# Kernel optimization log

Hardware: AMD Instinct MI355X
Metric: run time of the kernel (lower is better)

## Reference

```python
import jax, jax.numpy as jnp
import numpy as np

N = 262144
C = 256
G = 4096  # number of segments (upper bound on group ids)


def setup_inputs() -> dict:
    key = jax.random.key(0)
    ks = jax.random.split(key, 8)
    s = 1.0 / np.sqrt(C)
    x = jax.random.normal(ks[0], (1, N, C), dtype=jnp.float32)
    ix = jax.random.randint(ks[1], (N,), 0, G, dtype=jnp.int64)
    Wf = jax.random.uniform(ks[2], (C, C), jnp.float32, -s, s)
    bf = jax.random.uniform(ks[3], (C,), jnp.float32, -s, s)
    Wg = jax.random.uniform(ks[4], (C, C), jnp.float32, -s, s)
    bg = jax.random.uniform(ks[5], (C,), jnp.float32, -s, s)
    Wh = jax.random.uniform(ks[6], (C, C), jnp.float32, -s, s)
    bh = jax.random.uniform(ks[7], (C,), jnp.float32, -s, s)
    return {"x": x, "Wf": Wf, "bf": bf, "Wg": Wg, "bg": bg, "Wh": Wh, "bh": bh, "ix": ix}


def reference(x, Wf, bf, Wg, bg, Wh, bh, ix):
    # x: [1, N, C]; only batch 0 is used (matches torch module)
    x0 = x[0]                                    # [N, C]
    fx = x0 @ Wf.T + bf                          # [N, C]
    gx = jnp.clip(x0 @ Wg.T + bg, -50.0, 50.0)   # [N, C]
    exp_gx = jnp.exp(gx)                         # [N, C]
    # Segment softmax: sorting + cumsum group relabel in the torch code is
    # mathematically just a per-group normalized weighted sum keyed by ix.
    seg = ix.astype(jnp.int32)
    denom = jax.ops.segment_sum(exp_gx, seg, num_segments=G)   # [G, C]
    w = exp_gx / denom[seg]                                    # [N, C]
    y = jax.ops.segment_sum(fx * w, seg, num_segments=G)       # [G, C]
    y = y @ Wh.T + bh                                          # [G, C]
    out = y[seg]                                               # [N, C]
    return out[None]                                           # [1, N, C]
```

## Files before the change

kernel.cpp:

```cpp
#include <hip/hip_runtime.h>
#include <stdint.h>
#include <stddef.h>

#define N_ROWS 262144
#define CCH    256
#define NGRP   4096

typedef short bf16x8 __attribute__((ext_vector_type(8)));
typedef short bf16x4 __attribute__((ext_vector_type(4)));
typedef float f32x4  __attribute__((ext_vector_type(4)));
typedef int   i32x4  __attribute__((ext_vector_type(4)));

static __device__ __forceinline__ short f2bf(float f){
  union { float f; unsigned u; } v; v.f = f;
  unsigned u = v.u;
  unsigned r = (u + 0x7FFFu + ((u >> 16) & 1u)) >> 16;
  return (short)r;
}

typedef __attribute__((address_space(1))) const unsigned int GU32;
typedef __attribute__((address_space(3))) unsigned int LU32;
static __device__ __forceinline__ void gload_lds16(const void* g, void* l){
  __builtin_amdgcn_global_load_lds((GU32*)g, (LU32*)l, 16, 0, 0);
}

__global__ __launch_bounds__(256) void k_castw(
    const float* __restrict__ Wf, const float* __restrict__ Wg,
    const float* __restrict__ Wh,
    short* __restrict__ wfb, short* __restrict__ wgb, float* __restrict__ wht)
{
  int e = blockIdx.x * 256 + threadIdx.x;
  wfb[e] = f2bf(Wf[e]);
  wgb[e] = f2bf(Wg[e]);
  int k = e >> 8, j = e & 255;
  wht[e] = Wh[j * 256 + k];
}

__global__ __launch_bounds__(256) void k_hist(const int* __restrict__ ix, int* __restrict__ counts){
  int i = blockIdx.x * blockDim.x + threadIdx.x;
  int stride = gridDim.x * blockDim.x;
  for (; i < N_ROWS; i += stride) atomicAdd(&counts[ix[i]], 1);
}

__global__ __launch_bounds__(1024) void k_scan(const int* __restrict__ counts, int* __restrict__ cursor){
  __shared__ int sums[1024];
  int t = threadIdx.x;
  int base = t * 4;
  int c0 = counts[base], c1 = counts[base+1], c2 = counts[base+2], c3 = counts[base+3];
  sums[t] = c0 + c1 + c2 + c3;
  __syncthreads();
  for (int off = 1; off < 1024; off <<= 1){
    int v = (t >= off) ? sums[t - off] : 0;
    __syncthreads();
    sums[t] += v;
    __syncthreads();
  }
  int prev = (t == 0) ? 0 : sums[t - 1];
  cursor[base]   = prev;
  cursor[base+1] = prev + c0;
  cursor[base+2] = prev + c0 + c1;
  cursor[base+3] = prev + c0 + c1 + c2;
}

__global__ __launch_bounds__(256) void k_scatter(const int* __restrict__ ix, int* __restrict__ cursor,
                                                 int* __restrict__ order, int* __restrict__ gid){
  int i = blockIdx.x * blockDim.x + threadIdx.x;
  int stride = gridDim.x * blockDim.x;
  for (; i < N_ROWS; i += stride){
    int g = ix[i];
    int p = atomicAdd(&cursor[g], 1);
    order[p] = i;
    gid[p] = g;
  }
}

__global__ __launch_bounds__(256) void k_gemm(
    const float* __restrict__ x,
    const short* __restrict__ wfb, const short* __restrict__ wgb,
    const float* __restrict__ bfp, const float* __restrict__ bgp,
    const int* __restrict__ order, const int* __restrict__ gid,
    float* __restrict__ numer, float* __restrict__ denom)
{
  __shared__ short bst[2][2][8][512];
  __shared__ int ord_s[128];
  __shared__ int gid_s[128];

  const int tid  = threadIdx.x;
  const int wave = tid >> 6;
  const int lane = tid & 63;
  const int l16  = lane & 15;
  const int quad = lane >> 4;

  const int r0 = blockIdx.x * 128;
  const int j0 = blockIdx.y * 128;

  if (tid < 128){ ord_s[tid] = order[r0 + tid]; gid_s[tid] = gid[r0 + tid]; }
  __syncthreads();

  const float* xr0 = x + (size_t)ord_s[wave * 32 + l16] * 256;
  const float* xr1 = x + (size_t)ord_s[wave * 32 + 16 + l16] * 256;

  const int sm  = wave >> 1;
  const int sks = wave & 1;
  const short* wsrc = sm ? wgb : wfb;
  const short* bsrc = wsrc + (size_t)(j0 + l16) * 256 + sks * 32 + quad * 8;

  f32x4 accF[2][8], accG[2][8];
  #pragma unroll
  for (int rg = 0; rg < 2; ++rg)
    #pragma unroll
    for (int t = 0; t < 8; ++t){
      accF[rg][t] = (f32x4){0.f,0.f,0.f,0.f};
      accG[rg][t] = (f32x4){0.f,0.f,0.f,0.f};
    }

  for (int kc = 0; kc < 4; ++kc){
    const int k0 = kc * 64;
    #pragma unroll
    for (int t = 0; t < 8; ++t)
      gload_lds16(bsrc + (size_t)t * 16 * 256 + k0, &bst[sm][sks][t][0]);
    f32x4 av[2][2][2];
    #pragma unroll
    for (int rg = 0; rg < 2; ++rg){
      const float* xp = (rg ? xr1 : xr0) + k0 + quad * 8;
      #pragma unroll
      for (int ks = 0; ks < 2; ++ks){
        av[rg][ks][0] = *(const f32x4*)(xp + ks * 32);
        av[rg][ks][1] = *(const f32x4*)(xp + ks * 32 + 4);
      }
    }
    __syncthreads();
    #pragma unroll
    for (int ks = 0; ks < 2; ++ks){
      bf16x8 a0, a1;
      #pragma unroll
      for (int j = 0; j < 4; ++j){
        a0[j]   = f2bf(av[0][ks][0][j]);
        a0[4+j] = f2bf(av[0][ks][1][j]);
        a1[j]   = f2bf(av[1][ks][0][j]);
        a1[4+j] = f2bf(av[1][ks][1][j]);
      }
      #pragma unroll
      for (int t = 0; t < 8; ++t){
        bf16x8 bFv = *(const bf16x8*)&bst[0][ks][t][lane * 8];
        accF[0][t] = __builtin_amdgcn_mfma_f32_16x16x32_bf16(a0, bFv, accF[0][t], 0, 0, 0);
        accF[1][t] = __builtin_amdgcn_mfma_f32_16x16x32_bf16(a1, bFv, accF[1][t], 0, 0, 0);
        bf16x8 bGv = *(const bf16x8*)&bst[1][ks][t][lane * 8];
        accG[0][t] = __builtin_amdgcn_mfma_f32_16x16x32_bf16(a0, bGv, accG[0][t], 0, 0, 0);
        accG[1][t] = __builtin_amdgcn_mfma_f32_16x16x32_bf16(a1, bGv, accG[1][t], 0, 0, 0);
      }
    }
    __syncthreads();
  }

  float bfr[8], bgr[8];
  #pragma unroll
  for (int t = 0; t < 8; ++t){
    bfr[t] = bfp[j0 + t * 16 + l16];
    bgr[t] = bgp[j0 + t * 16 + l16];
  }
  #pragma unroll
  for (int rg = 0; rg < 2; ++rg)
    #pragma unroll
    for (int t = 0; t < 8; ++t)
      #pragma unroll
      for (int r = 0; r < 4; ++r){
        float g = accG[rg][t][r] + bgr[t];
        g = fminf(fmaxf(g, -50.f), 50.f);
        float e = __expf(g);
        accF[rg][t][r] = (accF[rg][t][r] + bfr[t]) * e;
        accG[rg][t][r] = e;
      }

  const int base = wave * 32;
  const int qd4 = quad * 4;
  int start = 0;
  while (start < 32){
    int g = gid_s[base + start];
    int end = start + 1;
    while (end < 32 && gid_s[base + end] == g) ++end;
    #pragma unroll
    for (int t = 0; t < 8; ++t){
      float sF = 0.f, sE = 0.f;
      #pragma unroll
      for (int rg = 0; rg < 2; ++rg)
        #pragma unroll
        for (int r = 0; r < 4; ++r){
          int rl = rg * 16 + qd4 + r;
          bool in = (rl >= start) && (rl < end);
          sF += in ? accF[rg][t][r] : 0.f;
          sE += in ? accG[rg][t][r] : 0.f;
        }
      sF += __shfl_xor(sF, 16); sF += __shfl_xor(sF, 32);
      sE += __shfl_xor(sE, 16); sE += __shfl_xor(sE, 32);
      if (quad == 0){
        atomicAdd(&numer[(size_t)g * 256 + j0 + t * 16 + l16], sF);
        atomicAdd(&denom[(size_t)g * 256 + j0 + t * 16 + l16], sE);
      }
    }
    start = end;
  }
}

__global__ __launch_bounds__(256) void k_yh(
    const float* __restrict__ numer, const float* __restrict__ denom,
    const float* __restrict__ wht, const float* __restrict__ bh,
    float* __restrict__ yh)
{
  __shared__ float ys[16][256];
  int t = threadIdx.x;
  int g0 = blockIdx.x * 16;
  #pragma unroll
  for (int gg = 0; gg < 16; ++gg){
    size_t idx = (size_t)(g0 + gg) * 256 + t;
    float d = denom[idx];
    ys[gg][t] = (d != 0.f) ? (numer[idx] / d) : 0.f;
  }
  __syncthreads();
  float acc[16];
  #pragma unroll
  for (int gg = 0; gg < 16; ++gg) acc[gg] = 0.f;
  for (int k = 0; k < 256; k += 4){
    float w0 = wht[(k+0) * 256 + t];
    float w1 = wht[(k+1) * 256 + t];
    float w2 = wht[(k+2) * 256 + t];
    float w3 = wht[(k+3) * 256 + t];
    #pragma unroll
    for (int gg = 0; gg < 16; ++gg)
      acc[gg] += w0 * ys[gg][k] + w1 * ys[gg][k+1] + w2 * ys[gg][k+2] + w3 * ys[gg][k+3];
  }
  float b = bh[t];
  #pragma unroll
  for (int gg = 0; gg < 16; ++gg) yh[(size_t)(g0 + gg) * 256 + t] = acc[gg] + b;
}

__global__ __launch_bounds__(256) void k_out(const int* __restrict__ ix,
    const float* __restrict__ yh, float* __restrict__ out)
{
  int wave = threadIdx.x >> 6;
  int lane = threadIdx.x & 63;
  int i = blockIdx.x * 4 + wave;
  int stride = gridDim.x * 4;
  for (; i < N_ROWS; i += stride){
    int g = ix[i];
    f32x4 v = *(const f32x4*)(yh + (size_t)g * 256 + lane * 4);
    *(f32x4*)(out + (size_t)i * 256 + lane * 4) = v;
  }
}

extern "C" void kernel_launch(void* const* d_in, const int* in_sizes, int n_in,
                              void* d_out, int out_size, void* d_ws, size_t ws_size,
                              hipStream_t stream)
{
  const float* x  = (const float*)d_in[0];
  const float* Wf = (const float*)d_in[1];
  const float* bf = (const float*)d_in[2];
  const float* Wg = (const float*)d_in[3];
  const float* bg = (const float*)d_in[4];
  const float* Wh = (const float*)d_in[5];
  const float* bh = (const float*)d_in[6];
  const int*   ix = (const int*)d_in[7];
  float* out = (float*)d_out;

  char* ws = (char*)d_ws;
  float* numer  = (float*)(ws + 0);
  float* denom  = (float*)(ws + 4194304);
  int*   counts = (int*)  (ws + 8388608);
  int*   cursor = (int*)  (ws + 8404992);
  float* yh     = (float*)(ws + 8421376);
  float* wht    = (float*)(ws + 12615680);
  short* wfb    = (short*)(ws + 12877824);
  short* wgb    = (short*)(ws + 13008896);
  int*   order  = (int*)  (ws + 13139968);
  int*   gid    = (int*)  (ws + 14188544);

  hipMemsetAsync(ws, 0, 8404992, stream);

  k_castw<<<256, 256, 0, stream>>>(Wf, Wg, Wh, wfb, wgb, wht);
  k_hist<<<512, 256, 0, stream>>>(ix, counts);
  k_scan<<<1, 1024, 0, stream>>>(counts, cursor);
  k_scatter<<<512, 256, 0, stream>>>(ix, cursor, order, gid);
  dim3 ggrid(2048, 2);
  k_gemm<<<ggrid, 256, 0, stream>>>(x, wfb, wgb, bf, bg, order, gid, numer, denom);
  k_yh<<<256, 256, 0, stream>>>(numer, denom, wht, bh, yh);
  k_out<<<2048, 256, 0, stream>>>(ix, yh, out);
}
```

Baseline: 850.7 us.

## Fuse row permutation with bf16 cast and make GEMM persistent with resident weights

The scatter kernel now writes each x row, already cast to bf16, into its sorted position in a scratch buffer that reuses the output allocation. The GEMM then reads contiguous bf16 rows instead of gathering fp32 rows through an index array. The GEMM becomes persistent: 512-thread blocks each keep a 64-column slice of both weight matrices in LDS for the whole run and loop over row tiles, which removes the per-k-chunk weight reloads and barriers. In exchange there is an extra pass writing the bf16 copy of x, plus more blocks hitting the same atomics, and correctness depends on k_out fully overwriting the output buffer afterwards.

Result: slower. 1.060 ms (+24.7%).

```diff
diff --git a/kernel.cpp b/kernel.cpp
--- a/kernel.cpp
+++ b/kernel.cpp
@@ -9,7 +9,6 @@
 typedef short bf16x8 __attribute__((ext_vector_type(8)));
 typedef short bf16x4 __attribute__((ext_vector_type(4)));
 typedef float f32x4  __attribute__((ext_vector_type(4)));
-typedef int   i32x4  __attribute__((ext_vector_type(4)));
 
 static __device__ __forceinline__ short f2bf(float f){
   union { float f; unsigned u; } v; v.f = f;
@@ -62,28 +61,36 @@
   cursor[base+3] = prev + c0 + c1 + c2;
 }
 
-__global__ __launch_bounds__(256) void k_scatter(const int* __restrict__ ix, int* __restrict__ cursor,
-                                                 int* __restrict__ order, int* __restrict__ gid){
-  int i = blockIdx.x * blockDim.x + threadIdx.x;
-  int stride = gridDim.x * blockDim.x;
+__global__ __launch_bounds__(256) void k_scatter_cast(
+    const int* __restrict__ ix, int* __restrict__ cursor,
+    const float* __restrict__ x, short* __restrict__ xb, int* __restrict__ gid)
+{
+  int wave = threadIdx.x >> 6;
+  int lane = threadIdx.x & 63;
+  int i = blockIdx.x * 4 + wave;
+  int stride = gridDim.x * 4;
   for (; i < N_ROWS; i += stride){
     int g = ix[i];
-    int p = atomicAdd(&cursor[g], 1);
-    order[p] = i;
-    gid[p] = g;
-  }
-}
-
-__global__ __launch_bounds__(256) void k_gemm(
-    const float* __restrict__ x,
+    int p;
+    if (lane == 0) p = atomicAdd(&cursor[g], 1);
+    p = __shfl(p, 0);
+    f32x4 v = *(const f32x4*)(x + (size_t)i * 256 + lane * 4);
+    bf16x4 b;
+    #pragma unroll
+    for (int j = 0; j < 4; ++j) b[j] = f2bf(v[j]);
+    *(bf16x4*)(xb + (size_t)p * 256 + lane * 4) = b;
+    if (lane == 0) gid[p] = g;
+  }
+}
+
+__global__ __launch_bounds__(512, 4) void k_gemm(
+    const short* __restrict__ xb,
     const short* __restrict__ wfb, const short* __restrict__ wgb,
     const float* __restrict__ bfp, const float* __restrict__ bgp,
-    const int* __restrict__ order, const int* __restrict__ gid,
+    const int* __restrict__ gid,
     float* __restrict__ numer, float* __restrict__ denom)
 {
-  __shared__ short bst[2][2][8][512];
-  __shared__ int ord_s[128];
-  __shared__ int gid_s[128];
+  __shared__ short bst[64][512];
 
   const int tid  = threadIdx.x;
   const int wave = tid >> 6;
@@ -91,114 +98,105 @@
   const int l16  = lane & 15;
   const int quad = lane >> 4;
 
-  const int r0 = blockIdx.x * 128;
-  const int j0 = blockIdx.y * 128;
-
-  if (tid < 128){ ord_s[tid] = order[r0 + tid]; gid_s[tid] = gid[r0 + tid]; }
+  const int cg    = blockIdx.x & 3;
+  const int bslot = blockIdx.x >> 2;
+  const int j0    = cg * 64;
+
+  #pragma unroll
+  for (int q = 0; q < 8; ++q){
+    int f = wave * 8 + q;
+    int mat = f >> 5, ks = (f >> 2) & 7, t = f & 3;
+    const short* wsrc = mat ? wgb : wfb;
+    const short* src = wsrc + (size_t)(j0 + t * 16 + l16) * 256 + ks * 32 + quad * 8;
+    gload_lds16(src, &bst[f][0]);
+  }
   __syncthreads();
 
-  const float* xr0 = x + (size_t)ord_s[wave * 32 + l16] * 256;
-  const float* xr1 = x + (size_t)ord_s[wave * 32 + 16 + l16] * 256;
-
-  const int sm  = wave >> 1;
-  const int sks = wave & 1;
-  const short* wsrc = sm ? wgb : wfb;
-  const short* bsrc = wsrc + (size_t)(j0 + l16) * 256 + sks * 32 + quad * 8;
-
-  f32x4 accF[2][8], accG[2][8];
-  #pragma unroll
-  for (int rg = 0; rg < 2; ++rg)
-    #pragma unroll
-    for (int t = 0; t < 8; ++t){
-      accF[rg][t] = (f32x4){0.f,0.f,0.f,0.f};
-      accG[rg][t] = (f32x4){0.f,0.f,0.f,0.f};
-    }
-
-  for (int kc = 0; kc < 4; ++kc){
-    const int k0 = kc * 64;
-    #pragma unroll
-    for (int t = 0; t < 8; ++t)
-      gload_lds16(bsrc + (size_t)t * 16 * 256 + k0, &bst[sm][sks][t][0]);
-    f32x4 av[2][2][2];
-    #pragma unroll
-    for (int rg = 0; rg < 2; ++rg){
-      const float* xp = (rg ? xr1 : xr0) + k0 + quad * 8;
-      #pragma unroll
-      for (int ks = 0; ks < 2; ++ks){
-        av[rg][ks][0] = *(const f32x4*)(xp + ks * 32);
-        av[rg][ks][1] = *(const f32x4*)(xp + ks * 32 + 4);
-      }
-    }
-    __syncthreads();
-    #pragma unroll
-    for (int ks = 0; ks < 2; ++ks){
-      bf16x8 a0, a1;
-      #pragma unroll
-      for (int j = 0; j < 4; ++j){
-        a0[j]   = f2bf(av[0][ks][0][j]);
-        a0[4+j] = f2bf(av[0][ks][1][j]);
-        a1[j]   = f2bf(av[1][ks][0][j]);
-        a1[4+j] = f2bf(av[1][ks][1][j]);
-      }
-      #pragma unroll
-      for (int t = 0; t < 8; ++t){
-        bf16x8 bFv = *(const bf16x8*)&bst[0][ks][t][lane * 8];
-        accF[0][t] = __builtin_amdgcn_mfma_f32_16x16x32_bf16(a0, bFv, accF[0][t], 0, 0, 0);
-        accF[1][t] = __builtin_amdgcn_mfma_f32_16x16x32_bf16(a1, bFv, accF[1][t], 0, 0, 0);
-        bf16x8 bGv = *(const bf16x8*)&bst[1][ks][t][lane * 8];
-        accG[0][t] = __builtin_amdgcn_mfma_f32_16x16x32_bf16(a0, bGv, accG[0][t], 0, 0, 0);
-        accG[1][t] = __builtin_amdgcn_mfma_f32_16x16x32_bf16(a1, bGv, accG[1][t], 0, 0, 0);
-      }
-    }
-    __syncthreads();
-  }
-
-  float bfr[8], bgr[8];
-  #pragma unroll
-  for (int t = 0; t < 8; ++t){
+  float bfr[4], bgr[4];
+  #pragma unroll
+  for (int t = 0; t < 4; ++t){
     bfr[t] = bfp[j0 + t * 16 + l16];
     bgr[t] = bgp[j0 + t * 16 + l16];
   }
-  #pragma unroll
-  for (int rg = 0; rg < 2; ++rg)
-    #pragma unroll
-    for (int t = 0; t < 8; ++t)
-      #pragma unroll
-      for (int r = 0; r < 4; ++r){
-        float g = accG[rg][t][r] + bgr[t];
-        g = fminf(fmaxf(g, -50.f), 50.f);
-        float e = __expf(g);
-        accF[rg][t][r] = (accF[rg][t][r] + bfr[t]) * e;
-        accG[rg][t][r] = e;
+
+  for (int tile = bslot; tile < N_ROWS / 256; tile += 128){
+    const int row0 = tile * 256 + wave * 32;
+    const int gidv = gid[row0 + (lane & 31)];
+    const short* xr0 = xb + (size_t)(row0 + l16) * 256 + quad * 8;
+    const short* xr1 = xr0 + 16 * 256;
+
+    f32x4 accF[2][4], accG[2][4];
+    #pragma unroll
+    for (int rg = 0; rg < 2; ++rg)
+      #pragma unroll
+      for (int t = 0; t < 4; ++t){
+        accF[rg][t] = (f32x4){0.f,0.f,0.f,0.f};
+        accG[rg][t] = (f32x4){0.f,0.f,0.f,0.f};
       }
 
-  const int base = wave * 32;
-  const int qd4 = quad * 4;
-  int start = 0;
-  while (start < 32){
-    int g = gid_s[base + start];
-    int end = start + 1;
-    while (end < 32 && gid_s[base + end] == g) ++end;
-    #pragma unroll
-    for (int t = 0; t < 8; ++t){
-      float sF = 0.f, sE = 0.f;
-      #pragma unroll
-      for (int rg = 0; rg < 2; ++rg)
+    #pragma unroll
+    for (int kc = 0; kc < 4; ++kc){
+      bf16x8 a[2][2];
+      a[0][0] = *(const bf16x8*)(xr0 + kc * 64);
+      a[0][1] = *(const bf16x8*)(xr0 + kc * 64 + 32);
+      a[1][0] = *(const bf16x8*)(xr1 + kc * 64);
+      a[1][1] = *(const bf16x8*)(xr1 + kc * 64 + 32);
+      __builtin_amdgcn_s_setprio(1);
+      #pragma unroll
+      for (int ks = 0; ks < 2; ++ks){
+        const int kk = kc * 2 + ks;
+        #pragma unroll
+        for (int t = 0; t < 4; ++t){
+          bf16x8 bF = *(const bf16x8*)&bst[kk * 4 + t][lane * 8];
+          accF[0][t] = __builtin_amdgcn_mfma_f32_16x16x32_bf16(a[0][ks], bF, accF[0][t], 0, 0, 0);
+          accF[1][t] = __builtin_amdgcn_mfma_f32_16x16x32_bf16(a[1][ks], bF, accF[1][t], 0, 0, 0);
+          bf16x8 bG = *(const bf16x8*)&bst[32 + kk * 4 + t][lane * 8];
+          accG[0][t] = __builtin_amdgcn_mfma_f32_16x16x32_bf16(a[0][ks], bG, accG[0][t], 0, 0, 0);
+          accG[1][t] = __builtin_amdgcn_mfma_f32_16x16x32_bf16(a[1][ks], bG, accG[1][t], 0, 0, 0);
+        }
+      }
+      __builtin_amdgcn_s_setprio(0);
+    }
+
+    #pragma unroll
+    for (int rg = 0; rg < 2; ++rg)
+      #pragma unroll
+      for (int t = 0; t < 4; ++t)
         #pragma unroll
         for (int r = 0; r < 4; ++r){
-          int rl = rg * 16 + qd4 + r;
-          bool in = (rl >= start) && (rl < end);
-          sF += in ? accF[rg][t][r] : 0.f;
-          sE += in ? accG[rg][t][r] : 0.f;
+          float g = accG[rg][t][r] + bgr[t];
+          g = fminf(fmaxf(g, -50.f), 50.f);
+          float e = __expf(g);
+          accF[rg][t][r] = (accF[rg][t][r] + bfr[t]) * e;
+          accG[rg][t][r] = e;
         }
-      sF += __shfl_xor(sF, 16); sF += __shfl_xor(sF, 32);
-      sE += __shfl_xor(sE, 16); sE += __shfl_xor(sE, 32);
-      if (quad == 0){
-        atomicAdd(&numer[(size_t)g * 256 + j0 + t * 16 + l16], sF);
-        atomicAdd(&denom[(size_t)g * 256 + j0 + t * 16 + l16], sE);
+
+    int start = 0;
+    while (start < 32){
+      int g = __shfl(gidv, start);
+      int end = start + 1;
+      while (end < 32 && __shfl(gidv, end) == g) ++end;
+      #pragma unroll
+      for (int t = 0; t < 4; ++t){
+        float sF = 0.f, sE = 0.f;
+        #pragma unroll
+        for (int rg = 0; rg < 2; ++rg)
+          #pragma unroll
+          for (int r = 0; r < 4; ++r){
+            int rl = rg * 16 + quad * 4 + r;
+            bool in = (rl >= start) && (rl < end);
+            sF += in ? accF[rg][t][r] : 0.f;
+            sE += in ? accG[rg][t][r] : 0.f;
+          }
+        sF += __shfl_xor(sF, 16); sF += __shfl_xor(sF, 32);
+        sE += __shfl_xor(sE, 16); sE += __shfl_xor(sE, 32);
+        if (quad == 0){
+          atomicAdd(&numer[(size_t)g * 256 + j0 + t * 16 + l16], sF);
+          atomicAdd(&denom[(size_t)g * 256 + j0 + t * 16 + l16], sE);
+        }
       }
+      start = end;
     }
-    start = end;
   }
 }
 
@@ -271,17 +269,17 @@
   float* wht    = (float*)(ws + 12615680);
   short* wfb    = (short*)(ws + 12877824);
   short* wgb    = (short*)(ws + 13008896);
-  int*   order  = (int*)  (ws + 13139968);
-  int*   gid    = (int*)  (ws + 14188544);
+  int*   gid    = (int*)  (ws + 13139968);
+
+  short* xb = (short*)d_out;
 
   hipMemsetAsync(ws, 0, 8404992, stream);
 
   k_castw<<<256, 256, 0, stream>>>(Wf, Wg, Wh, wfb, wgb, wht);
   k_hist<<<512, 256, 0, stream>>>(ix, counts);
   k_scan<<<1, 1024, 0, stream>>>(counts, cursor);
-  k_scatter<<<512, 256, 0, stream>>>(ix, cursor, order, gid);
-  dim3 ggrid(2048, 2);
-  k_gemm<<<ggrid, 256, 0, stream>>>(x, wfb, wgb, bf, bg, order, gid, numer, denom);
+  k_scatter_cast<<<2048, 256, 0, stream>>>(ix, cursor, x, xb, gid);
+  k_gemm<<<512, 512, 0, stream>>>(xb, wfb, wgb, bf, bg, gid, numer, denom);
   k_yh<<<256, 256, 0, stream>>>(numer, denom, wht, bh, yh);
   k_out<<<2048, 256, 0, stream>>>(ix, yh, out);
 }
```
